# Optimization experiments

Measured on AMD Instinct MI355X. Metric: run time of the kernel, lower is better.

Reference implementation:

```python
import jax, jax.numpy as jnp
import numpy as np

TEMPERATURE = 8.0  # sqrt(d_k=64)
MASK_FILL = -1e10


def setup_inputs() -> dict:
    key = jax.random.key(0)
    kq, kk, kv, km = jax.random.split(key, 4)
    b, lq, lk, dk, dv = 32, 2048, 2048, 64, 64
    q = jax.random.normal(kq, (b, lq, dk), dtype=jnp.float32)
    k = jax.random.normal(kk, (b, lk, dk), dtype=jnp.float32)
    v = jax.random.normal(kv, (b, lk, dv), dtype=jnp.float32)
    mask = jax.random.randint(km, (b, lq, lk), 0, 2).astype(jnp.bool_)
    return {"q": q, "k": k, "v": v, "mask": mask}


def reference(q, k, v, mask):
    # attn = q @ k^T / temperature, masked_fill, softmax over keys (dim=2)
    attn = jnp.einsum("bqd,bkd->bqk", q, k) / TEMPERATURE
    attn = jnp.where(mask, MASK_FILL, attn)
    attn = jax.nn.softmax(attn, axis=2)
    # dropout p=0.0 (eval/deterministic reference) -> identity
    output = jnp.einsum("bqk,bkv->bqv", attn, v)
    return (output, attn)
```

## Files before the change

kernel.cpp:

```cpp
#include <hip/hip_runtime.h>
#include <cstdint>
#include <cstddef>

#define B_   32
#define LQ   2048
#define LK   2048
#define DK   64
#define DV   64
#define TQ   16
#define LDP  2056

typedef short bf16x8 __attribute__((ext_vector_type(8)));
typedef float f32x4  __attribute__((ext_vector_type(4)));

#define KSCALE 0.1803368801111204f

__device__ __forceinline__ short f2bf(float f) {
  unsigned u = __builtin_bit_cast(unsigned, f);
  u += 0x7fffu + ((u >> 16) & 1u);
  return (short)(u >> 16);
}

__device__ __forceinline__ bf16x8 pack8(float4 a, float4 b) {
  bf16x8 r;
  r[0]=f2bf(a.x); r[1]=f2bf(a.y); r[2]=f2bf(a.z); r[3]=f2bf(a.w);
  r[4]=f2bf(b.x); r[5]=f2bf(b.y); r[6]=f2bf(b.z); r[7]=f2bf(b.w);
  return r;
}

__global__ __launch_bounds__(512, 4) void sdpa_kernel(
    const float* __restrict__ q, const float* __restrict__ k,
    const float* __restrict__ v, const int* __restrict__ mask,
    float* __restrict__ out, float* __restrict__ attn) {
  __shared__ short P[TQ][LDP];
  __shared__ float rowsum[TQ];
  __shared__ float rinv[TQ];

  const int tid  = threadIdx.x;
  const int wave = tid >> 6;
  const int lane = tid & 63;
  const int quad = lane >> 4;
  const int l15  = lane & 15;
  const int b     = blockIdx.y;
  const int qbase = blockIdx.x * TQ;

  if (tid < TQ) rowsum[tid] = 0.0f;
  __syncthreads();

  const float* qr = q + ((size_t)b * LQ + qbase + l15) * DK + quad * 8;
  bf16x8 qa0 = pack8(*(const float4*)(qr),      *(const float4*)(qr + 4));
  bf16x8 qa1 = pack8(*(const float4*)(qr + 32), *(const float4*)(qr + 36));

  const float* kbase = k + (size_t)b * LK * DK + (size_t)l15 * DK + quad * 8;
  const int*   mbase = mask + ((size_t)b * LQ + qbase + quad * 4) * (size_t)LK + l15;
  float*       abase = attn + ((size_t)b * LQ + qbase + quad * 4) * (size_t)LK + l15;
  const f32x4 z4 = {0.f, 0.f, 0.f, 0.f};

  float4 kp0, kp1, kp2, kp3;
  int mp0[4], mp1[4];
  {
    const float* kr = kbase + (size_t)wave * (16 * DK);
    kp0 = *(const float4*)(kr);      kp1 = *(const float4*)(kr + 4);
    kp2 = *(const float4*)(kr + 32); kp3 = *(const float4*)(kr + 36);
    const int* mr0 = mbase + wave * 16;
    const int* mr1 = mbase + (wave + 8) * 16;
    #pragma unroll
    for (int r = 0; r < 4; ++r) {
      mp0[r] = __builtin_nontemporal_load(mr0 + (size_t)r * LK);
      mp1[r] = __builtin_nontemporal_load(mr1 + (size_t)r * LK);
    }
  }
  float sum0[4] = {0,0,0,0};
  #pragma unroll 1
  for (int j = 0; j < 16; ++j) {
    float4 kc0 = kp0, kc1 = kp1, kc2 = kp2, kc3 = kp3;
    int mc[4];
    #pragma unroll
    for (int r = 0; r < 4; ++r) { mc[r] = mp0[r]; mp0[r] = mp1[r]; }
    const int ntc = wave + 8 * j;
    if (j < 15) {
      const float* kr = kbase + (size_t)(ntc + 8) * (16 * DK);
      kp0 = *(const float4*)(kr);      kp1 = *(const float4*)(kr + 4);
      kp2 = *(const float4*)(kr + 32); kp3 = *(const float4*)(kr + 36);
    }
    if (j < 14) {
      const int* mr = mbase + (ntc + 16) * 16;
      #pragma unroll
      for (int r = 0; r < 4; ++r)
        mp1[r] = __builtin_nontemporal_load(mr + (size_t)r * LK);
    }
    bf16x8 kb0 = pack8(kc0, kc1);
    bf16x8 kb1 = pack8(kc2, kc3);
    f32x4 acc0 = __builtin_amdgcn_mfma_f32_16x16x32_bf16(qa0, kb0, z4, 0, 0, 0);
    acc0       = __builtin_amdgcn_mfma_f32_16x16x32_bf16(qa1, kb1, acc0, 0, 0, 0);
    const int col = ntc * 16 + l15;
    float* ast = abase + ntc * 16;
    #pragma unroll
    for (int r = 0; r < 4; ++r) {
      float p = mc[r] ? 0.0f : __builtin_amdgcn_exp2f(acc0[r] * KSCALE);
      P[quad * 4 + r][col] = f2bf(p);
      ast[(size_t)r * LK] = p;
      sum0[r] += p;
    }
  }
  #pragma unroll
  for (int r = 0; r < 4; ++r) {
    float s0 = sum0[r];
    #pragma unroll
    for (int off = 1; off < 16; off <<= 1) s0 += __shfl_xor(s0, off);
    if (l15 == 0) atomicAdd(&rowsum[quad * 4 + r], s0);
  }
  __syncthreads();
  if (tid < TQ) rinv[tid] = 1.0f / rowsum[tid];
  __syncthreads();

  if (wave < 4) {
    const float* vbase = v + (size_t)b * LK * DV + wave * 16 + l15;
    f32x4 o0 = z4;
    float fva[8], fvb[8];
    #pragma unroll
    for (int j = 0; j < 8; ++j) {
      fva[j] = vbase[(size_t)(quad * 8 + j) * DV];
      fvb[j] = vbase[(size_t)(32 + quad * 8 + j) * DV];
    }
    #pragma unroll 1
    for (int kt = 0; kt < 64; kt += 2) {
      float fc[8];
      #pragma unroll
      for (int j = 0; j < 8; ++j) fc[j] = fva[j];
      if (kt != 62) {
        #pragma unroll
        for (int j = 0; j < 8; ++j)
          fva[j] = vbase[(size_t)((kt + 2) * 32 + quad * 8 + j) * DV];
      }
      bf16x8 bv0;
      #pragma unroll
      for (int j = 0; j < 8; ++j) bv0[j] = f2bf(fc[j]);
      bf16x8 a0 = *(const bf16x8*)&P[l15][kt * 32 + quad * 8];
      o0 = __builtin_amdgcn_mfma_f32_16x16x32_bf16(a0, bv0, o0, 0, 0, 0);

      #pragma unroll
      for (int j = 0; j < 8; ++j) fc[j] = fvb[j];
      if (kt != 62) {
        #pragma unroll
        for (int j = 0; j < 8; ++j)
          fvb[j] = vbase[(size_t)((kt + 3) * 32 + quad * 8 + j) * DV];
      }
      bf16x8 bv1;
      #pragma unroll
      for (int j = 0; j < 8; ++j) bv1[j] = f2bf(fc[j]);
      bf16x8 a1 = *(const bf16x8*)&P[l15][(kt + 1) * 32 + quad * 8];
      o0 = __builtin_amdgcn_mfma_f32_16x16x32_bf16(a1, bv1, o0, 0, 0, 0);
    }
    #pragma unroll
    for (int r = 0; r < 4; ++r) {
      const int row0 = quad * 4 + r;
      out[((size_t)b * LQ + qbase + row0) * DV + wave * 16 + l15] = o0[r] * rinv[row0];
    }
  } else {
    const int ww = wave - 4;
    float* arow = attn + ((size_t)b * LQ + qbase) * (size_t)LK + lane * 4;
    #pragma unroll 1
    for (int j = 0; j < 4; ++j) {
      const int row = ww * 4 + j;
      const float ri = rinv[row];
      float* dst = arow + (size_t)row * LK;
      f32x4 vals[8];
      #pragma unroll
      for (int it = 0; it < 8; ++it)
        vals[it] = *(const f32x4*)(dst + it * 256);
      #pragma unroll
      for (int it = 0; it < 8; ++it) {
        f32x4 vv = vals[it];
        vv[0] *= ri; vv[1] *= ri; vv[2] *= ri; vv[3] *= ri;
        *(f32x4*)(dst + it * 256) = vv;
      }
    }
  }
}

extern "C" void kernel_launch(void* const* d_in, const int* in_sizes, int n_in,
                              void* d_out, int out_size, void* d_ws, size_t ws_size,
                              hipStream_t stream) {
  (void)in_sizes; (void)n_in; (void)out_size; (void)d_ws; (void)ws_size;
  const float* q    = (const float*)d_in[0];
  const float* k    = (const float*)d_in[1];
  const float* v    = (const float*)d_in[2];
  const int*   mask = (const int*)d_in[3];
  float* out  = (float*)d_out;
  float* attn = out + (size_t)B_ * LQ * DV;
  dim3 grid(LQ / TQ, B_);
  sdpa_kernel<<<grid, 512, 0, stream>>>(q, k, v, mask, out, attn);
}
```

Baseline: 1.425 ms.

## Split into rowsum pass and recompute pass with bit-packed mask in output scratch

The single kernel becomes two. The first computes QK^T, builds row sums and packs the mask into ballot bitmasks, storing them in the output buffer, with the row sums kept in the first attn element of each row. The second kernel recomputes QK^T, normalises with the reciprocal row sums, writes attn once with nontemporal stores, and splits the PV product across all 8 waves, reducing the halves through shared memory. This removes the read-modify-write rescale of the huge attn matrix and the second full mask read, at the cost of recomputing QK^T and an extra launch.

```diff
diff --git a/kernel.cpp b/kernel.cpp
--- a/kernel.cpp
+++ b/kernel.cpp
@@ -28,16 +28,14 @@
   return r;
 }
 
-__global__ __launch_bounds__(512, 4) void sdpa_kernel(
+__global__ __launch_bounds__(512, 6) void rowsum_kernel(
     const float* __restrict__ q, const float* __restrict__ k,
-    const float* __restrict__ v, const int* __restrict__ mask,
-    float* __restrict__ out, float* __restrict__ attn) {
-  __shared__ short P[TQ][LDP];
+    const int* __restrict__ mask, float* __restrict__ bmout,
+    float* __restrict__ attn) {
   __shared__ float rowsum[TQ];
-  __shared__ float rinv[TQ];
 
   const int tid  = threadIdx.x;
-  const int wave = tid >> 6;
+  const int wv   = tid >> 6;
   const int lane = tid & 63;
   const int quad = lane >> 4;
   const int l15  = lane & 15;
@@ -53,17 +51,18 @@
 
   const float* kbase = k + (size_t)b * LK * DK + (size_t)l15 * DK + quad * 8;
   const int*   mbase = mask + ((size_t)b * LQ + qbase + quad * 4) * (size_t)LK + l15;
-  float*       abase = attn + ((size_t)b * LQ + qbase + quad * 4) * (size_t)LK + l15;
+  unsigned long long* bmbase =
+      (unsigned long long*)(bmout + ((size_t)b * LQ + qbase) * DV);
   const f32x4 z4 = {0.f, 0.f, 0.f, 0.f};
 
   float4 kp0, kp1, kp2, kp3;
   int mp0[4], mp1[4];
   {
-    const float* kr = kbase + (size_t)wave * (16 * DK);
+    const float* kr = kbase + (size_t)wv * (16 * DK);
     kp0 = *(const float4*)(kr);      kp1 = *(const float4*)(kr + 4);
     kp2 = *(const float4*)(kr + 32); kp3 = *(const float4*)(kr + 36);
-    const int* mr0 = mbase + wave * 16;
-    const int* mr1 = mbase + (wave + 8) * 16;
+    const int* mr0 = mbase + wv * 16;
+    const int* mr1 = mbase + (wv + 8) * 16;
     #pragma unroll
     for (int r = 0; r < 4; ++r) {
       mp0[r] = __builtin_nontemporal_load(mr0 + (size_t)r * LK);
@@ -77,7 +76,7 @@
     int mc[4];
     #pragma unroll
     for (int r = 0; r < 4; ++r) { mc[r] = mp0[r]; mp0[r] = mp1[r]; }
-    const int ntc = wave + 8 * j;
+    const int ntc = wv + 8 * j;
     if (j < 15) {
       const float* kr = kbase + (size_t)(ntc + 8) * (16 * DK);
       kp0 = *(const float4*)(kr);      kp1 = *(const float4*)(kr + 4);
@@ -88,6 +87,80 @@
       #pragma unroll
       for (int r = 0; r < 4; ++r)
         mp1[r] = __builtin_nontemporal_load(mr + (size_t)r * LK);
+    }
+    bf16x8 kb0 = pack8(kc0, kc1);
+    bf16x8 kb1 = pack8(kc2, kc3);
+    f32x4 acc0 = __builtin_amdgcn_mfma_f32_16x16x32_bf16(qa0, kb0, z4, 0, 0, 0);
+    acc0       = __builtin_amdgcn_mfma_f32_16x16x32_bf16(qa1, kb1, acc0, 0, 0, 0);
+    #pragma unroll
+    for (int r = 0; r < 4; ++r) {
+      const bool mm = (mc[r] != 0);
+      unsigned long long bal = __ballot(mm);
+      float p = mm ? 0.0f : __builtin_amdgcn_exp2f(acc0[r] * KSCALE);
+      sum0[r] += p;
+      if (lane == r) bmbase[(size_t)ntc * 4 + r] = bal;
+    }
+  }
+  #pragma unroll
+  for (int r = 0; r < 4; ++r) {
+    float s0 = sum0[r];
+    #pragma unroll
+    for (int off = 1; off < 16; off <<= 1) s0 += __shfl_xor(s0, off);
+    if (l15 == 0) atomicAdd(&rowsum[quad * 4 + r], s0);
+  }
+  __syncthreads();
+  if (tid < TQ)
+    attn[((size_t)b * LQ + qbase + tid) * (size_t)LK] = rowsum[tid];
+}
+
+__global__ __launch_bounds__(512, 4) void attn_pv_kernel(
+    const float* __restrict__ q, const float* __restrict__ k,
+    const float* __restrict__ v, float* out, float* attn) {
+  __shared__ short P[TQ][LDP];
+  __shared__ uint2 BM[512];
+  __shared__ float rinv[TQ];
+  __shared__ float Opart[TQ][68];
+
+  const int tid  = threadIdx.x;
+  const int wv   = tid >> 6;
+  const int lane = tid & 63;
+  const int quad = lane >> 4;
+  const int l15  = lane & 15;
+  const int b     = blockIdx.y;
+  const int qbase = blockIdx.x * TQ;
+
+  const uint2* bmg = (const uint2*)(out + ((size_t)b * LQ + qbase) * DV);
+  BM[tid] = bmg[tid];
+  if (tid < TQ)
+    rinv[tid] = 1.0f / attn[((size_t)b * LQ + qbase + tid) * (size_t)LK];
+  __syncthreads();
+
+  float my_ri[4];
+  #pragma unroll
+  for (int r = 0; r < 4; ++r) my_ri[r] = rinv[quad * 4 + r];
+
+  const float* qr = q + ((size_t)b * LQ + qbase + l15) * DK + quad * 8;
+  bf16x8 qa0 = pack8(*(const float4*)(qr),      *(const float4*)(qr + 4));
+  bf16x8 qa1 = pack8(*(const float4*)(qr + 32), *(const float4*)(qr + 36));
+
+  const float* kbase = k + (size_t)b * LK * DK + (size_t)l15 * DK + quad * 8;
+  float* abase = attn + ((size_t)b * LQ + qbase + quad * 4) * (size_t)LK + l15;
+  const f32x4 z4 = {0.f, 0.f, 0.f, 0.f};
+
+  float4 kp0, kp1, kp2, kp3;
+  {
+    const float* kr = kbase + (size_t)wv * (16 * DK);
+    kp0 = *(const float4*)(kr);      kp1 = *(const float4*)(kr + 4);
+    kp2 = *(const float4*)(kr + 32); kp3 = *(const float4*)(kr + 36);
+  }
+  #pragma unroll 1
+  for (int j = 0; j < 16; ++j) {
+    float4 kc0 = kp0, kc1 = kp1, kc2 = kp2, kc3 = kp3;
+    const int ntc = wv + 8 * j;
+    if (j < 15) {
+      const float* kr = kbase + (size_t)(ntc + 8) * (16 * DK);
+      kp0 = *(const float4*)(kr);      kp1 = *(const float4*)(kr + 4);
+      kp2 = *(const float4*)(kr + 32); kp3 = *(const float4*)(kr + 36);
     }
     bf16x8 kb0 = pack8(kc0, kc1);
     bf16x8 kb1 = pack8(kc2, kc3);
@@ -97,84 +170,69 @@
     float* ast = abase + ntc * 16;
     #pragma unroll
     for (int r = 0; r < 4; ++r) {
-      float p = mc[r] ? 0.0f : __builtin_amdgcn_exp2f(acc0[r] * KSCALE);
+      uint2 wm = BM[ntc * 4 + r];
+      unsigned ws = (lane & 32) ? wm.y : wm.x;
+      const bool mm = (ws >> (lane & 31)) & 1u;
+      float p = mm ? 0.0f
+                   : __builtin_amdgcn_exp2f(acc0[r] * KSCALE) * my_ri[r];
       P[quad * 4 + r][col] = f2bf(p);
-      ast[(size_t)r * LK] = p;
-      sum0[r] += p;
-    }
-  }
+      __builtin_nontemporal_store(p, ast + (size_t)r * LK);
+    }
+  }
+  __syncthreads();
+
+  const int w    = wv & 3;
+  const int half = wv >> 2;
+  const int ktb  = half * 32;
+  const float* vbase = v + (size_t)b * LK * DV + w * 16 + l15;
+  f32x4 o0 = z4;
+  float fva[8], fvb[8];
   #pragma unroll
-  for (int r = 0; r < 4; ++r) {
-    float s0 = sum0[r];
-    #pragma unroll
-    for (int off = 1; off < 16; off <<= 1) s0 += __shfl_xor(s0, off);
-    if (l15 == 0) atomicAdd(&rowsum[quad * 4 + r], s0);
-  }
-  __syncthreads();
-  if (tid < TQ) rinv[tid] = 1.0f / rowsum[tid];
-  __syncthreads();
-
-  if (wave < 4) {
-    const float* vbase = v + (size_t)b * LK * DV + wave * 16 + l15;
-    f32x4 o0 = z4;
-    float fva[8], fvb[8];
-    #pragma unroll
-    for (int j = 0; j < 8; ++j) {
-      fva[j] = vbase[(size_t)(quad * 8 + j) * DV];
-      fvb[j] = vbase[(size_t)(32 + quad * 8 + j) * DV];
-    }
-    #pragma unroll 1
-    for (int kt = 0; kt < 64; kt += 2) {
-      float fc[8];
+  for (int jj = 0; jj < 8; ++jj) {
+    fva[jj] = vbase[(size_t)(ktb * 32 + quad * 8 + jj) * DV];
+    fvb[jj] = vbase[(size_t)((ktb + 1) * 32 + quad * 8 + jj) * DV];
+  }
+  #pragma unroll 1
+  for (int kt2 = 0; kt2 < 32; kt2 += 2) {
+    const int kt = ktb + kt2;
+    float fc[8];
+    #pragma unroll
+    for (int jj = 0; jj < 8; ++jj) fc[jj] = fva[jj];
+    if (kt2 != 30) {
       #pragma unroll
-      for (int j = 0; j < 8; ++j) fc[j] = fva[j];
-      if (kt != 62) {
-        #pragma unroll
-        for (int j = 0; j < 8; ++j)
-          fva[j] = vbase[(size_t)((kt + 2) * 32 + quad * 8 + j) * DV];
-      }
-      bf16x8 bv0;
+      for (int jj = 0; jj < 8; ++jj)
+        fva[jj] = vbase[(size_t)((kt + 2) * 32 + quad * 8 + jj) * DV];
+    }
+    bf16x8 bv0;
+    #pragma unroll
+    for (int jj = 0; jj < 8; ++jj) bv0[jj] = f2bf(fc[jj]);
+    bf16x8 a0 = *(const bf16x8*)&P[l15][kt * 32 + quad * 8];
+    o0 = __builtin_amdgcn_mfma_f32_16x16x32_bf16(a0, bv0, o0, 0, 0, 0);
+
+    #pragma unroll
+    for (int jj = 0; jj < 8; ++jj) fc[jj] = fvb[jj];
+    if (kt2 != 30) {
       #pragma unroll
-      for (int j = 0; j < 8; ++j) bv0[j] = f2bf(fc[j]);
-      bf16x8 a0 = *(const bf16x8*)&P[l15][kt * 32 + quad * 8];
-      o0 = __builtin_amdgcn_mfma_f32_16x16x32_bf16(a0, bv0, o0, 0, 0, 0);
-
-      #pragma unroll
-      for (int j = 0; j < 8; ++j) fc[j] = fvb[j];
-      if (kt != 62) {
-        #pragma unroll
-        for (int j = 0; j < 8; ++j)
-          fvb[j] = vbase[(size_t)((kt + 3) * 32 + quad * 8 + j) * DV];
-      }
-      bf16x8 bv1;
-      #pragma unroll
-      for (int j = 0; j < 8; ++j) bv1[j] = f2bf(fc[j]);
-      bf16x8 a1 = *(const bf16x8*)&P[l15][(kt + 1) * 32 + quad * 8];
-      o0 = __builtin_amdgcn_mfma_f32_16x16x32_bf16(a1, bv1, o0, 0, 0, 0);
-    }
+      for (int jj = 0; jj < 8; ++jj)
+        fvb[jj] = vbase[(size_t)((kt + 3) * 32 + quad * 8 + jj) * DV];
+    }
+    bf16x8 bv1;
+    #pragma unroll
+    for (int jj = 0; jj < 8; ++jj) bv1[jj] = f2bf(fc[jj]);
+    bf16x8 a1 = *(const bf16x8*)&P[l15][(kt + 1) * 32 + quad * 8];
+    o0 = __builtin_amdgcn_mfma_f32_16x16x32_bf16(a1, bv1, o0, 0, 0, 0);
+  }
+  if (half == 1) {
+    #pragma unroll
+    for (int r = 0; r < 4; ++r) Opart[quad * 4 + r][w * 16 + l15] = o0[r];
+  }
+  __syncthreads();
+  if (half == 0) {
     #pragma unroll
     for (int r = 0; r < 4; ++r) {
       const int row0 = quad * 4 + r;
-      out[((size_t)b * LQ + qbase + row0) * DV + wave * 16 + l15] = o0[r] * rinv[row0];
-    }
-  } else {
-    const int ww = wave - 4;
-    float* arow = attn + ((size_t)b * LQ + qbase) * (size_t)LK + lane * 4;
-    #pragma unroll 1
-    for (int j = 0; j < 4; ++j) {
-      const int row = ww * 4 + j;
-      const float ri = rinv[row];
-      float* dst = arow + (size_t)row * LK;
-      f32x4 vals[8];
-      #pragma unroll
-      for (int it = 0; it < 8; ++it)
-        vals[it] = *(const f32x4*)(dst + it * 256);
-      #pragma unroll
-      for (int it = 0; it < 8; ++it) {
-        f32x4 vv = vals[it];
-        vv[0] *= ri; vv[1] *= ri; vv[2] *= ri; vv[3] *= ri;
-        *(f32x4*)(dst + it * 256) = vv;
-      }
+      out[((size_t)b * LQ + qbase + row0) * DV + w * 16 + l15] =
+          o0[r] + Opart[row0][w * 16 + l15];
     }
   }
 }
@@ -190,5 +248,6 @@
   float* out  = (float*)d_out;
   float* attn = out + (size_t)B_ * LQ * DV;
   dim3 grid(LQ / TQ, B_);
-  sdpa_kernel<<<grid, 512, 0, stream>>>(q, k, v, mask, out, attn);
-}
+  rowsum_kernel<<<grid, 512, 0, stream>>>(q, k, mask, out, attn);
+  attn_pv_kernel<<<grid, 512, 0, stream>>>(q, k, v, out, attn);
+}
```

Result: no change. 1.451 ms (+1.9%).
